# Optimization experiments

Hardware: AMD Instinct MI355X
Metric: run time of the kernel (lower is better)

## Reference

```python
import jax, jax.numpy as jnp
import numpy as np

B, N, E, D, H, O = 4, 10000, 160000, 128, 4, 64
NEG_SLOPE = 0.2  # PyG GATConv default


def setup_inputs() -> dict:
    key = jax.random.key(0)
    ks = jax.random.split(key, 9)
    x = jax.random.normal(ks[0], (B, N, D), jnp.float32)
    edge_index = jax.random.randint(ks[1], (2, E), 0, N, dtype=jnp.int64)
    edge_attr = jax.random.uniform(ks[2], (E,), jnp.float32)
    W_src = jax.random.normal(ks[3], (D, H, O), jnp.float32) * (1.0 / np.sqrt(D))
    att_src = jax.random.normal(ks[4], (H, O), jnp.float32) * 0.1
    att_dst = jax.random.normal(ks[5], (H, O), jnp.float32) * 0.1
    W_edge = jax.random.normal(ks[6], (H, O), jnp.float32) * 0.1  # lin_edge weight for edge_dim=1
    att_edge = jax.random.normal(ks[7], (H, O), jnp.float32) * 0.1
    bias = jnp.zeros((O,), jnp.float32)
    return {"x": x, "edge_index": edge_index, "edge_attr": edge_attr,
            "W_src": W_src, "att_src": att_src, "att_dst": att_dst,
            "W_edge": W_edge, "att_edge": att_edge, "bias": bias}


def reference(x, edge_index, edge_attr, W_src, att_src, att_dst, W_edge, att_edge, bias):
    src, dst = edge_index[0], edge_index[1]
    # shared linear projection (PyG non-bipartite GATConv): [B,N,H,O]
    h = jnp.einsum('bnd,dho->bnho', x, W_src)
    a_src = jnp.einsum('bnho,ho->bnh', h, att_src)  # [B,N,H]
    a_dst = jnp.einsum('bnho,ho->bnh', h, att_dst)  # [B,N,H]
    # edge feature projection (edge_dim=1): [E,H]
    a_edge = edge_attr[:, None] * jnp.einsum('ho,ho->h', W_edge, att_edge)[None, :]
    # attention logits per edge: [B,E,H]
    alpha = a_src[:, src] + a_dst[:, dst] + a_edge[None]
    alpha = jax.nn.leaky_relu(alpha, NEG_SLOPE)
    # segment softmax over destination nodes; segment ops need axis 0 = E
    alpha_t = jnp.transpose(alpha, (1, 0, 2))  # [E,B,H]
    m = jax.ops.segment_max(alpha_t, dst, num_segments=N)  # [N,B,H]
    m = jnp.where(jnp.isfinite(m), m, 0.0)
    p = jnp.exp(alpha_t - m[dst])
    s = jax.ops.segment_sum(p, dst, num_segments=N)
    w = p / jnp.maximum(s[dst], jnp.asarray(1e-16, p.dtype))  # [E,B,H]
    # weighted messages from source nodes, scatter-add into destinations
    msg = w[..., None] * jnp.transpose(h[:, src], (1, 0, 2, 3))  # [E,B,H,O]
    out = jax.ops.segment_sum(msg, dst, num_segments=N)  # [N,B,H,O]
    out = out.mean(axis=2) + bias  # concat=False -> mean over heads, [N,B,O]
    return jnp.transpose(out, (1, 0, 2))  # [B,N,O]
```

## Files before the change

### kernel.cpp

```cpp
#include <hip/hip_runtime.h>
#include <hip/hip_fp16.h>
#include <math.h>

constexpr int B_  = 4;
constexpr int N_  = 10000;
constexpr int E_  = 160000;
constexpr int D_  = 128;
constexpr int H_  = 4;
constexpr int O_  = 64;
constexpr float NEG_SLOPE = 0.2f;
constexpr int CAP = 64;
constexpr int GEMM_BLOCKS  = (B_ * N_) / 32;
constexpr int PLACE_BLOCKS = E_ / 256;

using half8   = __attribute__((ext_vector_type(8))) _Float16;
using half2v  = __attribute__((ext_vector_type(2))) _Float16;
using f32x4   = __attribute__((ext_vector_type(4))) float;
using ushort8v = __attribute__((ext_vector_type(8))) unsigned short;

static __device__ __forceinline__ unsigned short f2h(float f) {
    return __half_as_ushort(__float2half(f));
}
static __device__ __forceinline__ float h2f(unsigned short u) {
    return __half2float(__ushort_as_half(u));
}

#if __has_builtin(__builtin_amdgcn_fdot2)
#define FDOT2(a, b, c) __builtin_amdgcn_fdot2((a), (b), (c), false)
#else
static __device__ __forceinline__ float FDOT2(half2v a, half2v b, float c) {
    return c + (float)a[0] * (float)b[0] + (float)a[1] * (float)b[1];
}
#endif

__global__ __launch_bounds__(256) void k_prep(
    const float* __restrict__ Wsrc, const float* __restrict__ att_src,
    const float* __restrict__ att_dst,
    const float* __restrict__ W_edge, const float* __restrict__ att_edge,
    unsigned short* __restrict__ W1t, unsigned short* __restrict__ Vt,
    int* __restrict__ deg, float* __restrict__ c)
{
    const int d = blockIdx.x;
    const int t = threadIdx.x;
    const int h = t >> 6;

    for (int i = d * 256 + t; i < N_; i += 128 * 256) deg[i] = 0;

    const float wv = Wsrc[(size_t)d * 256 + t];
    const int cc = ((t & 63) << 2) | h;
    W1t[(size_t)cc * 128 + d] = f2h(wv);

    float vs = wv * att_src[t];
    float vd = wv * att_dst[t];
#pragma unroll
    for (int off = 32; off > 0; off >>= 1) {
        vs += __shfl_down(vs, off, 64);
        vd += __shfl_down(vd, off, 64);
    }
    if ((t & 63) == 0) {
        Vt[h * 128 + d]       = f2h(vs);
        Vt[(4 + h) * 128 + d] = f2h(vd);
    }
    if (d == 1) {
#pragma unroll
        for (int k = 0; k < 4; ++k) Vt[1024 + k * 256 + t] = 0;
    }

    if (d == 0) {
        float v = W_edge[t] * att_edge[t];
#pragma unroll
        for (int off = 32; off > 0; off >>= 1) v += __shfl_down(v, off, 64);
        if ((t & 63) == 0) c[h] = v;
    }
}

__global__ __launch_bounds__(256) void k_gemm(
    const float* __restrict__ x, const int* __restrict__ ei,
    const float* __restrict__ eattr,
    const unsigned short* __restrict__ W1t, const unsigned short* __restrict__ Vt,
    unsigned short* __restrict__ hbw, float* __restrict__ asrc, float* __restrict__ adst,
    int* __restrict__ deg, int2* __restrict__ srcea)
{
    constexpr int ROWS = 32;
    constexpr int APAD = 136;
    __shared__ uint4 SHq[1024];
    unsigned short* A1 = (unsigned short*)SHq;
    unsigned short* Cb = (unsigned short*)SHq;

    const int t = threadIdx.x;

    if (blockIdx.x >= GEMM_BLOCKS) {
        const int e = (blockIdx.x - GEMM_BLOCKS) * 256 + t;
        const int dstn = ei[E_ + e];
        const int r = atomicAdd(&deg[dstn], 1);
        srcea[dstn * CAP + r] = make_int2(ei[e], __float_as_int(eattr[e]));
        return;
    }

    const int w = t >> 6;
    const int lane = t & 63;
    const int i = lane & 15;
    const int q = lane >> 4;
    const size_t rowbase = (size_t)blockIdx.x * ROWS;

    half8 breg[4][4];
#pragma unroll
    for (int ks = 0; ks < 4; ++ks)
#pragma unroll
        for (int ctl = 0; ctl < 4; ++ctl) {
            const size_t boff = (size_t)((w * 4 + ctl) * 16 + i) * 128 + ks * 32 + q * 8;
            breg[ks][ctl] = *(const half8*)&W1t[boff];
        }
    half8 vreg[4];
    if (w < 2) {
#pragma unroll
        for (int ks = 0; ks < 4; ++ks)
            vreg[ks] = *(const half8*)&Vt[i * 128 + ks * 32 + q * 8];
    }

    {
        const float4* xg = (const float4*)(x + rowbase * D_);
#pragma unroll
        for (int it = 0; it < 4; ++it) {
            const int idx = it * 256 + t;
            const int row = idx >> 5;
            const int c4  = idx & 31;
            float4 xv = xg[idx];
            ushort4 h1;
            h1.x = f2h(xv.x); h1.y = f2h(xv.y);
            h1.z = f2h(xv.z); h1.w = f2h(xv.w);
            *(ushort4*)&A1[row * APAD + c4 * 4] = h1;
        }
    }
    __syncthreads();

    f32x4 acc[2][4];
#pragma unroll
    for (int tl = 0; tl < 2; ++tl)
#pragma unroll
        for (int ctl = 0; ctl < 4; ++ctl) acc[tl][ctl] = (f32x4){0.f, 0.f, 0.f, 0.f};
    f32x4 accV = (f32x4){0.f, 0.f, 0.f, 0.f};

#pragma unroll
    for (int ks = 0; ks < 4; ++ks) {
        const int a0off = i * APAD + ks * 32 + q * 8;
        const int a1off = (16 + i) * APAD + ks * 32 + q * 8;
        half8 at0 = *(const half8*)&A1[a0off];
        half8 at1 = *(const half8*)&A1[a1off];
#pragma unroll
        for (int ctl = 0; ctl < 4; ++ctl) {
            acc[0][ctl] = __builtin_amdgcn_mfma_f32_16x16x32_f16(at0, breg[ks][ctl], acc[0][ctl], 0, 0, 0);
            acc[1][ctl] = __builtin_amdgcn_mfma_f32_16x16x32_f16(at1, breg[ks][ctl], acc[1][ctl], 0, 0, 0);
        }
        if (w < 2) {
            const half8 atV = (w == 0) ? at0 : at1;
            accV = __builtin_amdgcn_mfma_f32_16x16x32_f16(atV, vreg[ks], accV, 0, 0, 0);
        }
    }

    if (w < 2 && i < 8) {
#pragma unroll
        for (int r = 0; r < 4; ++r) {
            const int row = w * 16 + q * 4 + r;
            const size_t rg = rowbase + row;
            if (i < 4) asrc[rg * 4 + i]       = accV[r];
            else       adst[rg * 4 + (i - 4)] = accV[r];
        }
    }

    __syncthreads();
#pragma unroll
    for (int tl = 0; tl < 2; ++tl) {
#pragma unroll
        for (int ctl = 0; ctl < 4; ++ctl) {
            const int col = (w * 4 + ctl) * 16 + i;
            const int chnk = col >> 3;
            const int within = col & 7;
#pragma unroll
            for (int r = 0; r < 4; ++r) {
                const int row = tl * 16 + q * 4 + r;
                const int s = chnk ^ row;
                Cb[row * 256 + s * 8 + within] = f2h(acc[tl][ctl][r]);
            }
        }
    }
    __syncthreads();
    {
        const int chnk = t & 31;
#pragma unroll
        for (int k = 0; k < 4; ++k) {
            const int row = k * 8 + (t >> 5);
            const int s = chnk ^ row;
            const uint4 v = *(const uint4*)&Cb[row * 256 + s * 8];
            *(uint4*)&hbw[(rowbase + row) * 256 + chnk * 8] = v;
        }
    }
}

__global__ __launch_bounds__(256) void k_agg(
    const int* __restrict__ deg, const int2* __restrict__ srcea,
    const float* __restrict__ asrc, const float* __restrict__ adst,
    const float* __restrict__ cvec, const unsigned short* __restrict__ hbu,
    const float* __restrict__ bias, float* __restrict__ out)
{
    __shared__ uint4 jS[4][64];

    const int b    = blockIdx.x & 3;
    const int g    = blockIdx.x >> 2;
    const int wave = threadIdx.x >> 6;
    const int lane = threadIdx.x & 63;
    const int dst  = g * 4 + wave;

    const int dg    = deg[dst];
    const int ebase = dst * CAP;

    const float4 ad = *(const float4*)&adst[((size_t)b * N_ + dst) * 4];
    const float4 cc = *(const float4*)cvec;

    const bool valid = lane < dg;
    const int2 rec = srcea[ebase + (valid ? lane : 0)];
    const int   srcl = valid ? rec.x : 0;
    const float ea   = __int_as_float(rec.y);
    const float4 as = *(const float4*)&asrc[((size_t)b * N_ + srcl) * 4];
    float4 al;
    al.x = as.x + ad.x + ea * cc.x;
    al.y = as.y + ad.y + ea * cc.y;
    al.z = as.z + ad.z + ea * cc.z;
    al.w = as.w + ad.w + ea * cc.w;
    al.x = al.x > 0.f ? al.x : NEG_SLOPE * al.x;
    al.y = al.y > 0.f ? al.y : NEG_SLOPE * al.y;
    al.z = al.z > 0.f ? al.z : NEG_SLOPE * al.z;
    al.w = al.w > 0.f ? al.w : NEG_SLOPE * al.w;
    float q0 = valid ? __expf(al.x) : 0.f;
    float q1 = valid ? __expf(al.y) : 0.f;
    float q2 = valid ? __expf(al.z) : 0.f;
    float q3 = valid ? __expf(al.w) : 0.f;
    const float px = q0, py = q1, pz = q2, pw = q3;

#pragma unroll
    for (int off = 32; off > 0; off >>= 1) {
        q0 += __shfl_xor(q0, off, 64);
        q1 += __shfl_xor(q1, off, 64);
        q2 += __shfl_xor(q2, off, 64);
        q3 += __shfl_xor(q3, off, 64);
    }
    const float i0 = 1.f / fmaxf(q0, 1e-16f);
    const float i1 = 1.f / fmaxf(q1, 1e-16f);
    const float i2 = 1.f / fmaxf(q2, 1e-16f);
    const float i3 = 1.f / fmaxf(q3, 1e-16f);

    union { half2v h; unsigned u; } u01, u23;
    u01.h[0] = (_Float16)(px * i0); u01.h[1] = (_Float16)(py * i1);
    u23.h[0] = (_Float16)(pz * i2); u23.h[1] = (_Float16)(pw * i3);
    jS[wave][lane] = make_uint4((unsigned)((b * N_ + srcl) << 8), u01.u, u23.u, 0u);
    __builtin_amdgcn_wave_barrier();

    const int half = lane >> 5;
    const int ol   = (lane & 31) * 8;

    float a0[4] = {0.f, 0.f, 0.f, 0.f};
    float a1[4] = {0.f, 0.f, 0.f, 0.f};

    for (int j = 0; j < dg; j += 8) {
#pragma unroll
        for (int u = 0; u < 4; ++u) {
            const int idx = j + 2 * u + half;
            const uint4 e4 = jS[wave][idx];
            const ushort8v hh = *(const ushort8v*)&hbu[(size_t)e4.x + ol];
            union { ushort8v s; half2v h[4]; } H; H.s = hh;
            union { unsigned u; half2v h; } p01, p23;
            p01.u = e4.y; p23.u = e4.z;
            a0[u] = FDOT2(H.h[0], p01.h, a0[u]);
            a0[u] = FDOT2(H.h[1], p23.h, a0[u]);
            a1[u] = FDOT2(H.h[2], p01.h, a1[u]);
            a1[u] = FDOT2(H.h[3], p23.h, a1[u]);
        }
    }

    float t0 = (a0[0] + a0[1]) + (a0[2] + a0[3]);
    float t1 = (a1[0] + a1[1]) + (a1[2] + a1[3]);
    t0 += __shfl_xor(t0, 32, 64);
    t1 += __shfl_xor(t1, 32, 64);

    if (lane < 32) {
        const float2 bs = *(const float2*)&bias[lane * 2];
        float2 res;
        res.x = 0.25f * t0 + bs.x;
        res.y = 0.25f * t1 + bs.y;
        *(float2*)&out[((size_t)b * N_ + dst) * O_ + lane * 2] = res;
    }
}

extern "C" void kernel_launch(void* const* d_in, const int* in_sizes, int n_in,
                              void* d_out, int out_size, void* d_ws, size_t ws_size,
                              hipStream_t stream)
{
    (void)in_sizes; (void)n_in; (void)out_size; (void)ws_size;
    const float* x        = (const float*)d_in[0];
    const int*   ei       = (const int*)d_in[1];
    const float* eattr    = (const float*)d_in[2];
    const float* Wsrc     = (const float*)d_in[3];
    const float* att_src  = (const float*)d_in[4];
    const float* att_dst  = (const float*)d_in[5];
    const float* W_edge   = (const float*)d_in[6];
    const float* att_edge = (const float*)d_in[7];
    const float* bias     = (const float*)d_in[8];
    float* out = (float*)d_out;

    char* w = (char*)d_ws;
    auto take = [&](size_t bytes) { char* p = w; w += (bytes + 15) & ~size_t(15); return p; };
    unsigned short* hb   = (unsigned short*)take((size_t)B_ * N_ * O_ * H_ * 2);
    float* asrc    = (float*)take((size_t)B_ * N_ * H_ * 4);
    float* adst    = (float*)take((size_t)B_ * N_ * H_ * 4);
    float* c       = (float*)take(4 * 4);
    unsigned short* W1t = (unsigned short*)take((size_t)256 * 128 * 2);
    unsigned short* Vt  = (unsigned short*)take((size_t)16 * 128 * 2);
    int* deg       = (int*)take((size_t)N_ * 4);
    int2* srcea    = (int2*)take((size_t)N_ * CAP * 8);

    hipLaunchKernelGGL(k_prep, dim3(128), dim3(256), 0, stream,
                       Wsrc, att_src, att_dst, W_edge, att_edge,
                       W1t, Vt, deg, c);
    hipLaunchKernelGGL(k_gemm, dim3(GEMM_BLOCKS + PLACE_BLOCKS), dim3(256), 0, stream,
                       x, ei, eattr, W1t, Vt, hb, asrc, adst, deg, srcea);
    hipLaunchKernelGGL(k_agg, dim3(N_ / 4 * B_), dim3(256), 0, stream,
                       deg, srcea, asrc, adst, c, hb, bias, out);
}
```

Measured before the change: 136.1 us.

## Process two 32-row tiles per GEMM block with prefetched x and staged overlap

Each GEMM block now handles 64 rows as two 32-row sub-tiles. Both tiles' x loads are issued up front into registers, and the second tile's fp16 conversion and LDS store overlap the first tile's epilogue. This amortizes the per-block weight-register loads (breg/vreg) over twice the rows and hides global load latency. The edge-placement blocks are moved to the front of the grid so their atomics start early. In exchange, LDS use and register pressure rise, and the grid has half as many GEMM blocks.

```diff
diff --git a/kernel.cpp b/kernel.cpp
--- a/kernel.cpp
+++ b/kernel.cpp
@@ -10,8 +10,8 @@
 constexpr int O_  = 64;
 constexpr float NEG_SLOPE = 0.2f;
 constexpr int CAP = 64;
-constexpr int GEMM_BLOCKS  = (B_ * N_) / 32;
 constexpr int PLACE_BLOCKS = E_ / 256;
+constexpr int GEMM_BLOCKS  = (B_ * N_) / 64;
 
 using half8   = __attribute__((ext_vector_type(8))) _Float16;
 using half2v  = __attribute__((ext_vector_type(2))) _Float16;
@@ -81,16 +81,16 @@
     unsigned short* __restrict__ hbw, float* __restrict__ asrc, float* __restrict__ adst,
     int* __restrict__ deg, int2* __restrict__ srcea)
 {
-    constexpr int ROWS = 32;
     constexpr int APAD = 136;
-    __shared__ uint4 SHq[1024];
-    unsigned short* A1 = (unsigned short*)SHq;
-    unsigned short* Cb = (unsigned short*)SHq;
+    __shared__ uint4 SHq[2112];
+    unsigned short* A0 = (unsigned short*)SHq;
+    unsigned short* A1 = (unsigned short*)SHq + 4352;
+    unsigned short* Cb = (unsigned short*)SHq + 8704;
 
     const int t = threadIdx.x;
 
-    if (blockIdx.x >= GEMM_BLOCKS) {
-        const int e = (blockIdx.x - GEMM_BLOCKS) * 256 + t;
+    if (blockIdx.x < PLACE_BLOCKS) {
+        const int e = blockIdx.x * 256 + t;
         const int dstn = ei[E_ + e];
         const int r = atomicAdd(&deg[dstn], 1);
         srcea[dstn * CAP + r] = make_int2(ei[e], __float_as_int(eattr[e]));
@@ -101,7 +101,14 @@
     const int lane = t & 63;
     const int i = lane & 15;
     const int q = lane >> 4;
-    const size_t rowbase = (size_t)blockIdx.x * ROWS;
+    const size_t rowbase = (size_t)(blockIdx.x - PLACE_BLOCKS) * 64;
+
+    const float4* xg = (const float4*)(x + rowbase * D_);
+    float4 xr0[4], xr1[4];
+#pragma unroll
+    for (int it = 0; it < 4; ++it) xr0[it] = xg[it * 256 + t];
+#pragma unroll
+    for (int it = 0; it < 4; ++it) xr1[it] = xg[1024 + it * 256 + t];
 
     half8 breg[4][4];
 #pragma unroll
@@ -118,28 +125,70 @@
             vreg[ks] = *(const half8*)&Vt[i * 128 + ks * 32 + q * 8];
     }
 
-    {
-        const float4* xg = (const float4*)(x + rowbase * D_);
-#pragma unroll
-        for (int it = 0; it < 4; ++it) {
-            const int idx = it * 256 + t;
-            const int row = idx >> 5;
-            const int c4  = idx & 31;
-            float4 xv = xg[idx];
-            ushort4 h1;
-            h1.x = f2h(xv.x); h1.y = f2h(xv.y);
-            h1.z = f2h(xv.z); h1.w = f2h(xv.w);
-            *(ushort4*)&A1[row * APAD + c4 * 4] = h1;
-        }
+#pragma unroll
+    for (int it = 0; it < 4; ++it) {
+        const int idx = it * 256 + t;
+        const int row = idx >> 5;
+        const int c4  = idx & 31;
+        ushort4 h1;
+        h1.x = f2h(xr0[it].x); h1.y = f2h(xr0[it].y);
+        h1.z = f2h(xr0[it].z); h1.w = f2h(xr0[it].w);
+        *(ushort4*)&A0[row * APAD + c4 * 4] = h1;
     }
     __syncthreads();
 
-    f32x4 acc[2][4];
+    f32x4 acc0[2][4];
 #pragma unroll
     for (int tl = 0; tl < 2; ++tl)
 #pragma unroll
-        for (int ctl = 0; ctl < 4; ++ctl) acc[tl][ctl] = (f32x4){0.f, 0.f, 0.f, 0.f};
-    f32x4 accV = (f32x4){0.f, 0.f, 0.f, 0.f};
+        for (int ctl = 0; ctl < 4; ++ctl) acc0[tl][ctl] = (f32x4){0.f, 0.f, 0.f, 0.f};
+    f32x4 accV0 = (f32x4){0.f, 0.f, 0.f, 0.f};
+
+#pragma unroll
+    for (int ks = 0; ks < 4; ++ks) {
+        const int a0off = i * APAD + ks * 32 + q * 8;
+        const int a1off = (16 + i) * APAD + ks * 32 + q * 8;
+        half8 at0 = *(const half8*)&A0[a0off];
+        half8 at1 = *(const half8*)&A0[a1off];
+#pragma unroll
+        for (int ctl = 0; ctl < 4; ++ctl) {
+            acc0[0][ctl] = __builtin_amdgcn_mfma_f32_16x16x32_f16(at0, breg[ks][ctl], acc0[0][ctl], 0, 0, 0);
+            acc0[1][ctl] = __builtin_amdgcn_mfma_f32_16x16x32_f16(at1, breg[ks][ctl], acc0[1][ctl], 0, 0, 0);
+        }
+        if (w < 2) {
+            const half8 atV = (w == 0) ? at0 : at1;
+            accV0 = __builtin_amdgcn_mfma_f32_16x16x32_f16(atV, vreg[ks], accV0, 0, 0, 0);
+        }
+    }
+
+#pragma unroll
+    for (int it = 0; it < 4; ++it) {
+        const int idx = it * 256 + t;
+        const int row = idx >> 5;
+        const int c4  = idx & 31;
+        ushort4 h1;
+        h1.x = f2h(xr1[it].x); h1.y = f2h(xr1[it].y);
+        h1.z = f2h(xr1[it].z); h1.w = f2h(xr1[it].w);
+        *(ushort4*)&A1[row * APAD + c4 * 4] = h1;
+    }
+
+    if (w < 2 && i < 8) {
+#pragma unroll
+        for (int r = 0; r < 4; ++r) {
+            const int row = w * 16 + q * 4 + r;
+            const size_t rg = rowbase + row;
+            if (i < 4) asrc[rg * 4 + i]       = accV0[r];
+            else       adst[rg * 4 + (i - 4)] = accV0[r];
+        }
+    }
+    __syncthreads();
+
+    f32x4 acc1[2][4];
+#pragma unroll
+    for (int tl = 0; tl < 2; ++tl)
+#pragma unroll
+        for (int ctl = 0; ctl < 4; ++ctl) acc1[tl][ctl] = (f32x4){0.f, 0.f, 0.f, 0.f};
+    f32x4 accV1 = (f32x4){0.f, 0.f, 0.f, 0.f};
 
 #pragma unroll
     for (int ks = 0; ks < 4; ++ks) {
@@ -149,26 +198,15 @@
         half8 at1 = *(const half8*)&A1[a1off];
 #pragma unroll
         for (int ctl = 0; ctl < 4; ++ctl) {
-            acc[0][ctl] = __builtin_amdgcn_mfma_f32_16x16x32_f16(at0, breg[ks][ctl], acc[0][ctl], 0, 0, 0);
-            acc[1][ctl] = __builtin_amdgcn_mfma_f32_16x16x32_f16(at1, breg[ks][ctl], acc[1][ctl], 0, 0, 0);
+            acc1[0][ctl] = __builtin_amdgcn_mfma_f32_16x16x32_f16(at0, breg[ks][ctl], acc1[0][ctl], 0, 0, 0);
+            acc1[1][ctl] = __builtin_amdgcn_mfma_f32_16x16x32_f16(at1, breg[ks][ctl], acc1[1][ctl], 0, 0, 0);
         }
         if (w < 2) {
             const half8 atV = (w == 0) ? at0 : at1;
-            accV = __builtin_amdgcn_mfma_f32_16x16x32_f16(atV, vreg[ks], accV, 0, 0, 0);
-        }
-    }
-
-    if (w < 2 && i < 8) {
-#pragma unroll
-        for (int r = 0; r < 4; ++r) {
-            const int row = w * 16 + q * 4 + r;
-            const size_t rg = rowbase + row;
-            if (i < 4) asrc[rg * 4 + i]       = accV[r];
-            else       adst[rg * 4 + (i - 4)] = accV[r];
-        }
-    }
-
-    __syncthreads();
+            accV1 = __builtin_amdgcn_mfma_f32_16x16x32_f16(atV, vreg[ks], accV1, 0, 0, 0);
+        }
+    }
+
 #pragma unroll
     for (int tl = 0; tl < 2; ++tl) {
 #pragma unroll
@@ -180,11 +218,22 @@
             for (int r = 0; r < 4; ++r) {
                 const int row = tl * 16 + q * 4 + r;
                 const int s = chnk ^ row;
-                Cb[row * 256 + s * 8 + within] = f2h(acc[tl][ctl][r]);
+                Cb[row * 256 + s * 8 + within] = f2h(acc0[tl][ctl][r]);
             }
         }
     }
+
+    if (w < 2 && i < 8) {
+#pragma unroll
+        for (int r = 0; r < 4; ++r) {
+            const int row = w * 16 + q * 4 + r;
+            const size_t rg = rowbase + 32 + row;
+            if (i < 4) asrc[rg * 4 + i]       = accV1[r];
+            else       adst[rg * 4 + (i - 4)] = accV1[r];
+        }
+    }
     __syncthreads();
+
     {
         const int chnk = t & 31;
 #pragma unroll
@@ -193,6 +242,35 @@
             const int s = chnk ^ row;
             const uint4 v = *(const uint4*)&Cb[row * 256 + s * 8];
             *(uint4*)&hbw[(rowbase + row) * 256 + chnk * 8] = v;
+        }
+    }
+    __syncthreads();
+
+#pragma unroll
+    for (int tl = 0; tl < 2; ++tl) {
+#pragma unroll
+        for (int ctl = 0; ctl < 4; ++ctl) {
+            const int col = (w * 4 + ctl) * 16 + i;
+            const int chnk = col >> 3;
+            const int within = col & 7;
+#pragma unroll
+            for (int r = 0; r < 4; ++r) {
+                const int row = tl * 16 + q * 4 + r;
+                const int s = chnk ^ row;
+                Cb[row * 256 + s * 8 + within] = f2h(acc1[tl][ctl][r]);
+            }
+        }
+    }
+    __syncthreads();
+
+    {
+        const int chnk = t & 31;
+#pragma unroll
+        for (int k = 0; k < 4; ++k) {
+            const int row = k * 8 + (t >> 5);
+            const int s = chnk ^ row;
+            const uint4 v = *(const uint4*)&Cb[row * 256 + s * 8];
+            *(uint4*)&hbw[(rowbase + 32 + row) * 256 + chnk * 8] = v;
         }
     }
 }
@@ -321,7 +399,7 @@
     hipLaunchKernelGGL(k_prep, dim3(128), dim3(256), 0, stream,
                        Wsrc, att_src, att_dst, W_edge, att_edge,
                        W1t, Vt, deg, c);
-    hipLaunchKernelGGL(k_gemm, dim3(GEMM_BLOCKS + PLACE_BLOCKS), dim3(256), 0, stream,
+    hipLaunchKernelGGL(k_gemm, dim3(PLACE_BLOCKS + GEMM_BLOCKS), dim3(256), 0, stream,
                        x, ei, eattr, W1t, Vt, hb, asrc, adst, deg, srcea);
     hipLaunchKernelGGL(k_agg, dim3(N_ / 4 * B_), dim3(256), 0, stream,
                        deg, srcea, asrc, adst, c, hb, bias, out);
```

New measurement: 133.9 us. About the same (-1.6%).
